# Kernel optimization log

Hardware: AMD Instinct MI355X
Metric: run time of the kernel (lower is better)

The kernel has to match this reference:

```python
import jax, jax.numpy as jnp
import numpy as np
import math


def setup_inputs() -> dict:
    key = jax.random.key(0)
    k_fm, k_x, k_y, k_w, k_h = jax.random.split(key, 5)
    C, H, W = 512, 256, 256
    N = 4096
    patch_num = 4
    pe = 2  # sqrt(patch_num)
    feature_map = jax.random.normal(k_fm, (C, H, W), dtype=jnp.float32)
    # Boxes fully inside the map with per-patch extent >= 2 so every sub-box is valid.
    min_wh = 2.0 * pe + 1.0
    x0 = jax.random.uniform(k_x, (N,), minval=0.0, maxval=W / 2 - 1.0)
    y0 = jax.random.uniform(k_y, (N,), minval=0.0, maxval=H / 2 - 1.0)
    w = jax.random.uniform(k_w, (N,), minval=min_wh, maxval=W / 2 - 2.0)
    h = jax.random.uniform(k_h, (N,), minval=min_wh, maxval=H / 2 - 2.0)
    roi_batch = jnp.stack([x0, y0, x0 + w, y0 + h], axis=1).astype(jnp.float32)
    return {"feature_map": feature_map, "roi_batch": roi_batch, "patch_num": patch_num}


def _box_indices(roi_batch, patch_num, W):
    """Rounded, clamped per-patch sub-box corners; shapes (P, N), flattened patch-major."""
    pe = int(math.isqrt(patch_num))
    xmin, ymin, xmax, ymax = (roi_batch[:, k] for k in range(4))
    i = jnp.arange(patch_num)
    ix = (i % pe).astype(roi_batch.dtype)[:, None]
    iy = (i // pe).astype(roi_batch.dtype)[:, None]
    ws = ((xmax - xmin) / pe)[None, :]
    hs = ((ymax - ymin) / pe)[None, :]
    ax = xmin[None, :] + ix * ws  # (P, N)
    ay = ymin[None, :] + iy * hs
    clampi = lambda v: jnp.clip(jnp.round(v), 0, W - 1).astype(jnp.int32)
    x0, x1 = clampi(ax), clampi(ax + ws)
    y0, y1 = clampi(ay), clampi(ay + hs)
    flat = lambda a: a.reshape(-1)  # loop order: patch outer, roi inner
    return flat(x0), flat(x1), flat(y0), flat(y1)


def reference(feature_map, roi_batch, patch_num):
    C, H, W = feature_map.shape
    x0, x1, y0, y1 = _box_indices(roi_batch, patch_num, W)
    cw = x1 - x0
    ch = y1 - y0
    mask = (cw >= 1) & (ch >= 1)  # (P*N,)
    # Integral image with zero row/col padding: S[:, y, x] = sum of fm[:, :y, :x]
    S = jnp.pad(jnp.cumsum(jnp.cumsum(feature_map, axis=1), axis=2),
                ((0, 0), (1, 0), (1, 0)))
    # Region sums via 4-corner gather: (C, B)
    sums = S[:, y1, x1] - S[:, y0, x1] - S[:, y1, x0] + S[:, y0, x0]
    area = jnp.maximum(cw * ch, 1).astype(feature_map.dtype)
    pooled = (sums / area).T  # (B, C) region means == adaptive_avg_pool2d(.,(1,1))
    pooled = pooled * mask.astype(feature_map.dtype)[:, None]
    return pooled[:, :, None, None], mask.astype(jnp.int32)
```

## Files before the change

kernel.cpp:

```cpp
#include <hip/hip_runtime.h>


#define CHN   512
#define HDIM  256
#define WDIM  256
#define SP    257

__global__ __launch_bounds__(256) void zeroK(float* __restrict__ S) {
    int gid = blockIdx.x * 256 + threadIdx.x;
    const int half = SP * CHN;
    if (gid < half) {
        S[gid] = 0.0f;
    } else {
        int g2 = gid - half;
        if (g2 < half) {
            int y = g2 >> 9;
            int c = g2 & 511;
            S[((size_t)y * SP) * CHN + c] = 0.0f;
        }
    }
}

__global__ __launch_bounds__(256) void rowScanK(const float* __restrict__ fm,
                                               float* __restrict__ S) {
    __shared__ float tile[32][SP];
    __shared__ double part[32][9];
    const int t  = threadIdx.x;
    const int y  = blockIdx.x;
    const int c0 = blockIdx.y * 32;

    {
        const int xr = (t & 63) * 4;
        const int cb = t >> 6;
        #pragma unroll
        for (int i = 0; i < 8; ++i) {
            const int c = i * 4 + cb;
            const float4 v = *(const float4*)(fm + ((size_t)(c0 + c) << 16)
                                                 + ((size_t)y << 8) + xr);
            tile[c][xr]     = v.x;
            tile[c][xr + 1] = v.y;
            tile[c][xr + 2] = v.z;
            tile[c][xr + 3] = v.w;
        }
    }
    __syncthreads();

    const int r = t & 31;
    const int s = t >> 5;
    {
        double a = 0.0;
        #pragma unroll 8
        for (int i = 0; i < 32; ++i) a += (double)tile[r][s * 32 + i];
        part[r][s] = a;
    }
    __syncthreads();
    if (t < 32) {
        double o = 0.0;
        #pragma unroll
        for (int ss = 0; ss < 8; ++ss) {
            double p = part[t][ss];
            part[t][ss] = o;
            o += p;
        }
    }
    __syncthreads();
    {
        double acc = part[r][s];
        #pragma unroll 8
        for (int i = 0; i < 32; ++i) {
            acc += (double)tile[r][s * 32 + i];
            tile[r][s * 32 + i] = (float)acc;
        }
    }
    __syncthreads();
    {
        #pragma unroll 4
        for (int it = 0; it < 32; ++it) {
            const int j   = it * 256 + t;
            const int cil = j & 31;
            const int x   = j >> 5;
            S[(((size_t)(y + 1)) * SP + (x + 1)) * CHN + (c0 + cil)] = tile[cil][x];
        }
    }
}

__global__ __launch_bounds__(256) void colScanK(float* __restrict__ S) {
    const int g = blockIdx.x * 256 + threadIdx.x;
    const int c = g & 511;
    const int x = (g >> 9) + 1;
    size_t idx = ((size_t)SP + x) * CHN + c;
    double acc = 0.0;
    #pragma unroll 4
    for (int yy = 1; yy <= HDIM; ++yy) {
        const float v = S[idx];
        acc += (double)v;
        S[idx] = (float)acc;
        idx += (size_t)SP * CHN;
    }
}

__global__ __launch_bounds__(256) void gatherK(const float* __restrict__ S,
                                              const float* __restrict__ roi,
                                              float* __restrict__ out,
                                              float* __restrict__ maskOut,
                                              int N) {
    const int b = blockIdx.x;
    const int n = b % N;
    const int p = b / N;

    const float xmin = roi[4 * n + 0];
    const float ymin = roi[4 * n + 1];
    const float xmax = roi[4 * n + 2];
    const float ymax = roi[4 * n + 3];

    const float ixf = (float)(p & 1);
    const float iyf = (float)(p >> 1);
    const float wsv = __fdiv_rn(__fsub_rn(xmax, xmin), 2.0f);
    const float hsv = __fdiv_rn(__fsub_rn(ymax, ymin), 2.0f);
    const float ax  = __fadd_rn(xmin, __fmul_rn(ixf, wsv));
    const float ay  = __fadd_rn(ymin, __fmul_rn(iyf, hsv));

    const float lim = (float)(WDIM - 1);
    float f;
    f = fminf(fmaxf(rintf(ax), 0.0f), lim);                     const int x0 = (int)f;
    f = fminf(fmaxf(rintf(__fadd_rn(ax, wsv)), 0.0f), lim);     const int x1 = (int)f;
    f = fminf(fmaxf(rintf(ay), 0.0f), lim);                     const int y0 = (int)f;
    f = fminf(fmaxf(rintf(__fadd_rn(ay, hsv)), 0.0f), lim);     const int y1 = (int)f;

    const int cw = x1 - x0;
    const int ch = y1 - y0;
    const int maskv = (cw >= 1 && ch >= 1) ? 1 : 0;
    int areai = cw * ch; if (areai < 1) areai = 1;
    const float areaf = (float)areai;
    const float maskf = (float)maskv;

    const float* p11 = S + ((size_t)y1 * SP + x1) * CHN;
    const float* p01 = S + ((size_t)y0 * SP + x1) * CHN;
    const float* p10 = S + ((size_t)y1 * SP + x0) * CHN;
    const float* p00 = S + ((size_t)y0 * SP + x0) * CHN;
    float* ob = out + (size_t)b * CHN;

    const int t = threadIdx.x;
    #pragma unroll
    for (int k = 0; k < 2; ++k) {
        const int c = t + k * 256;
        float v = ((p11[c] - p01[c]) - p10[c]) + p00[c];
        v = __fdiv_rn(v, areaf);
        ob[c] = v * maskf;
    }
    if (t == 0) maskOut[b] = maskf;
}

extern "C" void kernel_launch(void* const* d_in, const int* in_sizes, int n_in,
                              void* d_out, int out_size, void* d_ws, size_t ws_size,
                              hipStream_t stream) {
    const float* fm  = (const float*)d_in[0];
    const float* roi = (const float*)d_in[1];

    const int N = in_sizes[1] / 4;
    const int B = 4 * N;

    float* S       = (float*)d_ws;
    float* out     = (float*)d_out;
    float* maskOut = out + (size_t)B * CHN;

    zeroK<<<(2 * SP * CHN + 255) / 256, 256, 0, stream>>>(S);

    dim3 gA(HDIM, CHN / 32);
    rowScanK<<<gA, 256, 0, stream>>>(fm, S);

    colScanK<<<(WDIM * CHN) / 256, 256, 0, stream>>>(S);

    gatherK<<<B, 256, 0, stream>>>(S, roi, out, maskOut, N);
}
```

Baseline: 283.2 us.

## Use wave-shuffle row scan, prefetched column scan, and vectorized ROI gather

Replaces the shared-memory double-precision row scan with a per-wave shuffle prefix scan in float, and writes the integral image with float4 stores. The column scan now prefetches 16 rows into registers to hide load latency. The gather uses float4 loads with 128 threads per box and orders blocks ROI-major so the four patches of one ROI are adjacent. Float accumulation in the row scan may add rounding error compared with the double-based version.

```diff
diff --git a/kernel.cpp b/kernel.cpp
--- a/kernel.cpp
+++ b/kernel.cpp
@@ -5,6 +5,7 @@
 #define HDIM  256
 #define WDIM  256
 #define SP    257
+#define PADW  260
 
 __global__ __launch_bounds__(256) void zeroK(float* __restrict__ S) {
     int gid = blockIdx.x * 256 + threadIdx.x;
@@ -23,64 +24,46 @@
 
 __global__ __launch_bounds__(256) void rowScanK(const float* __restrict__ fm,
                                                float* __restrict__ S) {
-    __shared__ float tile[32][SP];
-    __shared__ double part[32][9];
-    const int t  = threadIdx.x;
-    const int y  = blockIdx.x;
-    const int c0 = blockIdx.y * 32;
+    __shared__ float tile[32][PADW];
+    const int t    = threadIdx.x;
+    const int lane = t & 63;
+    const int wave = t >> 6;
+    const int y    = blockIdx.x;
+    const int c0   = blockIdx.y * 32;
 
-    {
-        const int xr = (t & 63) * 4;
-        const int cb = t >> 6;
+    #pragma unroll
+    for (int cc = 0; cc < 8; ++cc) {
+        const int c = wave * 8 + cc;
+        const float4 v = *(const float4*)(fm + ((size_t)(c0 + c) << 16)
+                                             + ((size_t)y << 8) + 4 * lane);
+        const float local = ((v.x + v.y) + v.z) + v.w;
+        float s = local;
         #pragma unroll
-        for (int i = 0; i < 8; ++i) {
-            const int c = i * 4 + cb;
-            const float4 v = *(const float4*)(fm + ((size_t)(c0 + c) << 16)
-                                                 + ((size_t)y << 8) + xr);
-            tile[c][xr]     = v.x;
-            tile[c][xr + 1] = v.y;
-            tile[c][xr + 2] = v.z;
-            tile[c][xr + 3] = v.w;
+        for (int d = 1; d < 64; d <<= 1) {
+            float u = __shfl_up(s, d, 64);
+            if (lane >= d) s += u;
         }
+        const float e  = s - local;
+        float4 p;
+        p.x = e   + v.x;
+        p.y = p.x + v.y;
+        p.z = p.y + v.z;
+        p.w = p.z + v.w;
+        *(float4*)&tile[c][4 * lane] = p;
     }
     __syncthreads();
 
-    const int r = t & 31;
-    const int s = t >> 5;
-    {
-        double a = 0.0;
-        #pragma unroll 8
-        for (int i = 0; i < 32; ++i) a += (double)tile[r][s * 32 + i];
-        part[r][s] = a;
-    }
-    __syncthreads();
-    if (t < 32) {
-        double o = 0.0;
-        #pragma unroll
-        for (int ss = 0; ss < 8; ++ss) {
-            double p = part[t][ss];
-            part[t][ss] = o;
-            o += p;
-        }
-    }
-    __syncthreads();
-    {
-        double acc = part[r][s];
-        #pragma unroll 8
-        for (int i = 0; i < 32; ++i) {
-            acc += (double)tile[r][s * 32 + i];
-            tile[r][s * 32 + i] = (float)acc;
-        }
-    }
-    __syncthreads();
-    {
-        #pragma unroll 4
-        for (int it = 0; it < 32; ++it) {
-            const int j   = it * 256 + t;
-            const int cil = j & 31;
-            const int x   = j >> 5;
-            S[(((size_t)(y + 1)) * SP + (x + 1)) * CHN + (c0 + cil)] = tile[cil][x];
-        }
+    #pragma unroll
+    for (int it = 0; it < 8; ++it) {
+        const int lin = it * 256 + t;
+        const int cg  = lin & 7;
+        const int x   = lin >> 3;
+        float4 o;
+        o.x = tile[cg * 4 + 0][x];
+        o.y = tile[cg * 4 + 1][x];
+        o.z = tile[cg * 4 + 2][x];
+        o.w = tile[cg * 4 + 3][x];
+        *(float4*)(S + (((size_t)(y + 1)) * SP + (x + 1)) * CHN + c0 + cg * 4) = o;
     }
 }
 
@@ -88,25 +71,40 @@
     const int g = blockIdx.x * 256 + threadIdx.x;
     const int c = g & 511;
     const int x = (g >> 9) + 1;
+    const size_t stride = (size_t)SP * CHN;
     size_t idx = ((size_t)SP + x) * CHN + c;
+
+    float buf[16];
+    #pragma unroll
+    for (int i = 0; i < 16; ++i) buf[i] = S[idx + (size_t)i * stride];
+
     double acc = 0.0;
-    #pragma unroll 4
-    for (int yy = 1; yy <= HDIM; ++yy) {
-        const float v = S[idx];
-        acc += (double)v;
-        S[idx] = (float)acc;
-        idx += (size_t)SP * CHN;
+    for (int yb = 0; yb < 16; ++yb) {
+        float nbuf[16];
+        const size_t nidx = idx + 16 * stride;
+        if (yb < 15) {
+            #pragma unroll
+            for (int i = 0; i < 16; ++i) nbuf[i] = S[nidx + (size_t)i * stride];
+        }
+        #pragma unroll
+        for (int i = 0; i < 16; ++i) {
+            acc += (double)buf[i];
+            S[idx + (size_t)i * stride] = (float)acc;
+        }
+        idx = nidx;
+        #pragma unroll
+        for (int i = 0; i < 16; ++i) buf[i] = nbuf[i];
     }
 }
 
-__global__ __launch_bounds__(256) void gatherK(const float* __restrict__ S,
+__global__ __launch_bounds__(128) void gatherK(const float* __restrict__ S,
                                               const float* __restrict__ roi,
                                               float* __restrict__ out,
                                               float* __restrict__ maskOut,
                                               int N) {
-    const int b = blockIdx.x;
-    const int n = b % N;
-    const int p = b / N;
+    const int n = blockIdx.x >> 2;
+    const int p = blockIdx.x & 3;
+    const int b = p * N + n;
 
     const float xmin = roi[4 * n + 0];
     const float ymin = roi[4 * n + 1];
@@ -134,20 +132,24 @@
     const float areaf = (float)areai;
     const float maskf = (float)maskv;
 
-    const float* p11 = S + ((size_t)y1 * SP + x1) * CHN;
-    const float* p01 = S + ((size_t)y0 * SP + x1) * CHN;
-    const float* p10 = S + ((size_t)y1 * SP + x0) * CHN;
-    const float* p00 = S + ((size_t)y0 * SP + x0) * CHN;
-    float* ob = out + (size_t)b * CHN;
+    const float4* p11 = (const float4*)(S + ((size_t)y1 * SP + x1) * CHN);
+    const float4* p01 = (const float4*)(S + ((size_t)y0 * SP + x1) * CHN);
+    const float4* p10 = (const float4*)(S + ((size_t)y1 * SP + x0) * CHN);
+    const float4* p00 = (const float4*)(S + ((size_t)y0 * SP + x0) * CHN);
+    float4* ob = (float4*)(out + (size_t)b * CHN);
 
     const int t = threadIdx.x;
-    #pragma unroll
-    for (int k = 0; k < 2; ++k) {
-        const int c = t + k * 256;
-        float v = ((p11[c] - p01[c]) - p10[c]) + p00[c];
-        v = __fdiv_rn(v, areaf);
-        ob[c] = v * maskf;
-    }
+    const float4 a = p11[t];
+    const float4 bq = p01[t];
+    const float4 cq = p10[t];
+    const float4 dq = p00[t];
+    float4 o;
+    o.x = __fdiv_rn(((a.x - bq.x) - cq.x) + dq.x, areaf) * maskf;
+    o.y = __fdiv_rn(((a.y - bq.y) - cq.y) + dq.y, areaf) * maskf;
+    o.z = __fdiv_rn(((a.z - bq.z) - cq.z) + dq.z, areaf) * maskf;
+    o.w = __fdiv_rn(((a.w - bq.w) - cq.w) + dq.w, areaf) * maskf;
+    ob[t] = o;
+
     if (t == 0) maskOut[b] = maskf;
 }
 
@@ -171,5 +173,5 @@
 
     colScanK<<<(WDIM * CHN) / 256, 256, 0, stream>>>(S);
 
-    gatherK<<<B, 256, 0, stream>>>(S, roi, out, maskOut, N);
+    gatherK<<<B, 128, 0, stream>>>(S, roi, out, maskOut, N);
 }
```

New measurement: 284.0 us. About the same (+0.3%).
